# Performance work log

Hardware: AMD Instinct MI355X
Metric: run time of the kernel (lower is better)

Reference implementation:

```python
import jax, jax.numpy as jnp
import numpy as np

N_NODES = 50000


def sage_conv(x, src, dst, Wl, bl, Wr):
    # PyG SAGEConv (aggr='mean'): out = lin_l(mean_{j in N(i)} x_j) + lin_r(x_i)
    # lin_l has bias, lin_r (root) has no bias.
    n = x.shape[0]
    agg = jax.ops.segment_sum(x[src], dst, num_segments=n)          # [N, d_in]
    cnt = jax.ops.segment_sum(jnp.ones((src.shape[0],), x.dtype), dst, num_segments=n)
    mean = agg / jnp.maximum(cnt, 1.0)[:, None]
    return mean @ Wl + bl + x @ Wr


def setup_inputs() -> dict:
    key = jax.random.key(0)
    k1, k2, k3, k4, k5, k6, k7 = jax.random.split(key, 7)
    in_c, hid_c, out_c = 128, 128, 2
    x = jax.random.normal(k1, (N_NODES, in_c), dtype=jnp.float32)
    edge_index = jax.random.randint(k2, (2, 800000), 0, N_NODES, dtype=jnp.int64)
    s1 = 1.0 / np.sqrt(in_c)
    s2 = 1.0 / np.sqrt(hid_c)
    return {
        "x": x,
        "edge_index": edge_index,
        "W1l": jax.random.uniform(k3, (in_c, hid_c), jnp.float32, -s1, s1),
        "b1l": jnp.zeros((hid_c,), jnp.float32),
        "W1r": jax.random.uniform(k4, (in_c, hid_c), jnp.float32, -s1, s1),
        "W2l": jax.random.uniform(k5, (hid_c, out_c), jnp.float32, -s2, s2),
        "b2l": jnp.zeros((out_c,), jnp.float32),
        "W2r": jax.random.uniform(k6, (hid_c, out_c), jnp.float32, -s2, s2),
    }


def reference(x, edge_index, W1l, b1l, W1r, W2l, b2l, W2r):
    src, dst = edge_index[0], edge_index[1]
    h = jax.nn.relu(sage_conv(x, src, dst, W1l, b1l, W1r))
    return sage_conv(h, src, dst, W2l, b2l, W2r)
```

## Files before the change

### kernel.cpp

```cpp
#include <hip/hip_runtime.h>

#define N_NODES 50000
#define N_PAD 50176
#define N_EDGES 800000
#define C 128
#define CAP 48
#define NB 196
#define CBCAP 4608
#define B1_BUCK 391
#define TOBF_B 6250
#define PACK_B 16

typedef unsigned short ushort_t;
typedef unsigned int uint_t;
typedef __attribute__((ext_vector_type(8))) short bf16x8;
typedef __attribute__((ext_vector_type(4))) float f32x4;

__device__ __forceinline__ uint_t f2bf(float f) {
    uint_t u = __float_as_uint(f);
    u += 0x7fffu + ((u >> 16) & 1u);
    return u >> 16;
}
__device__ __forceinline__ float bflo(uint_t u) { return __uint_as_float(u << 16); }
__device__ __forceinline__ float bfhi(uint_t u) { return __uint_as_float(u & 0xffff0000u); }

__global__ __launch_bounds__(256) void bucket1_kernel(
    const int* __restrict__ src, const int* __restrict__ dst,
    int* __restrict__ gcur, int2* __restrict__ cb,
    const float* __restrict__ x, ushort_t* __restrict__ xh) {
    int b = blockIdx.x;
    if (b < B1_BUCK) {
        __shared__ int hist[NB];
        __shared__ int offs[NB];
        int t = threadIdx.x;
        if (t < NB) hist[t] = 0;
        __syncthreads();
        int tid = b * 256 + t;
        bool act = tid < N_EDGES / 8;
        int4 s0, s1, d0, d1;
        if (act) {
            s0 = ((const int4*)src)[2 * tid];
            s1 = ((const int4*)src)[2 * tid + 1];
            d0 = ((const int4*)dst)[2 * tid];
            d1 = ((const int4*)dst)[2 * tid + 1];
            atomicAdd(&hist[d0.x >> 8], 1);
            atomicAdd(&hist[d0.y >> 8], 1);
            atomicAdd(&hist[d0.z >> 8], 1);
            atomicAdd(&hist[d0.w >> 8], 1);
            atomicAdd(&hist[d1.x >> 8], 1);
            atomicAdd(&hist[d1.y >> 8], 1);
            atomicAdd(&hist[d1.z >> 8], 1);
            atomicAdd(&hist[d1.w >> 8], 1);
        }
        __syncthreads();
        if (t < NB) {
            offs[t] = atomicAdd(&gcur[t], hist[t]);
            hist[t] = 0;
        }
        __syncthreads();
        if (act) {
            int ss[8] = {s0.x, s0.y, s0.z, s0.w, s1.x, s1.y, s1.z, s1.w};
            int dd[8] = {d0.x, d0.y, d0.z, d0.w, d1.x, d1.y, d1.z, d1.w};
            #pragma unroll
            for (int i = 0; i < 8; i++) {
                int bkt = dd[i] >> 8;
                int pos = offs[bkt] + atomicAdd(&hist[bkt], 1);
                if (pos < CBCAP) cb[bkt * CBCAP + pos] = make_int2(ss[i], dd[i]);
            }
        }
    } else {
        int i = (b - B1_BUCK) * 256 + threadIdx.x;
        float4 v = ((const float4*)x)[i];
        uint_t lo = f2bf(v.x) | (f2bf(v.y) << 16);
        uint_t hi = f2bf(v.z) | (f2bf(v.w) << 16);
        ((uint2*)xh)[i] = make_uint2(lo, hi);
    }
}

__global__ __launch_bounds__(256) void bucket2_kernel(
    const int* __restrict__ gcur, const int2* __restrict__ cb,
    int* __restrict__ cursor, int* __restrict__ epad,
    const float* __restrict__ W1l, const float* __restrict__ W1r,
    ushort_t* __restrict__ Bp) {
    int b = blockIdx.x;
    if (b < NB) {
        __shared__ int cnt[256];
        int t = threadIdx.x;
        cnt[t] = 0;
        __syncthreads();
        int lenr = gcur[b];
        int len = lenr < CBCAP ? lenr : CBCAP;
        const int2* run = cb + b * CBCAP;
        for (int e = t; e < len; e += 256) {
            int2 sd = run[e];
            int pos = atomicAdd(&cnt[sd.y & 255], 1);
            if (pos < CAP) epad[sd.y * CAP + pos] = sd.x;
        }
        __syncthreads();
        int node = b * 256 + t;
        if (node < N_NODES) cursor[node] = cnt[t];
    } else {
        int p = (b - NB) * 256 + threadIdx.x;
        int lane = p & 63;
        int pair = p >> 6;
        int kk = pair & 7;
        int nt = pair >> 3;
        int n = lane & 15, quad = lane >> 4;
        int col = nt * 16 + n;
        int k0 = kk * 32 + quad * 8;
        uint_t w[4];
        #pragma unroll
        for (int jj = 0; jj < 4; jj++) {
            int ka = k0 + 2 * jj, kb = k0 + 2 * jj + 1;
            float fa = (ka < C) ? W1l[ka * C + col] : W1r[(ka - C) * C + col];
            float fb = (kb < C) ? W1l[kb * C + col] : W1r[(kb - C) * C + col];
            w[jj] = f2bf(fa) | (f2bf(fb) << 16);
        }
        ((uint4*)(Bp + (size_t)p * 8))[0] = make_uint4(w[0], w[1], w[2], w[3]);
    }
}

__device__ __forceinline__ void bf8_acc(float* a, const uint4 v) {
    a[0] += bflo(v.x); a[1] += bfhi(v.x);
    a[2] += bflo(v.y); a[3] += bfhi(v.y);
    a[4] += bflo(v.z); a[5] += bfhi(v.z);
    a[6] += bflo(v.w); a[7] += bfhi(v.w);
}

__global__ __launch_bounds__(256) void gather_kernel(const ushort_t* __restrict__ xh,
                                                     const int* __restrict__ cursor,
                                                     const int* __restrict__ epad,
                                                     ushort_t* __restrict__ msb) {
    int t = threadIdx.x;
    int slot = t >> 4, q = t & 15;
    int node = blockIdx.x * 16 + slot;
    int d = cursor[node];
    int dd = d < CAP ? d : CAP;
    const int* lst = epad + node * CAP;
    float a[8] = {0,0,0,0,0,0,0,0};
    float b[8] = {0,0,0,0,0,0,0,0};
    int e = 0;
    for (; e + 8 <= dd; e += 8) {
        int s0 = lst[e + 0], s1 = lst[e + 1], s2 = lst[e + 2], s3 = lst[e + 3];
        int s4 = lst[e + 4], s5 = lst[e + 5], s6 = lst[e + 6], s7 = lst[e + 7];
        uint4 v0 = ((const uint4*)(xh + (size_t)s0 * C))[q];
        uint4 v1 = ((const uint4*)(xh + (size_t)s1 * C))[q];
        uint4 v2 = ((const uint4*)(xh + (size_t)s2 * C))[q];
        uint4 v3 = ((const uint4*)(xh + (size_t)s3 * C))[q];
        uint4 v4 = ((const uint4*)(xh + (size_t)s4 * C))[q];
        uint4 v5 = ((const uint4*)(xh + (size_t)s5 * C))[q];
        uint4 v6 = ((const uint4*)(xh + (size_t)s6 * C))[q];
        uint4 v7 = ((const uint4*)(xh + (size_t)s7 * C))[q];
        bf8_acc(a, v0); bf8_acc(b, v1); bf8_acc(a, v2); bf8_acc(b, v3);
        bf8_acc(a, v4); bf8_acc(b, v5); bf8_acc(a, v6); bf8_acc(b, v7);
    }
    for (; e + 4 <= dd; e += 4) {
        int s0 = lst[e + 0], s1 = lst[e + 1], s2 = lst[e + 2], s3 = lst[e + 3];
        uint4 v0 = ((const uint4*)(xh + (size_t)s0 * C))[q];
        uint4 v1 = ((const uint4*)(xh + (size_t)s1 * C))[q];
        uint4 v2 = ((const uint4*)(xh + (size_t)s2 * C))[q];
        uint4 v3 = ((const uint4*)(xh + (size_t)s3 * C))[q];
        bf8_acc(a, v0); bf8_acc(b, v1); bf8_acc(a, v2); bf8_acc(b, v3);
    }
    for (; e < dd; e++) {
        uint4 v = ((const uint4*)(xh + (size_t)lst[e] * C))[q];
        bf8_acc(a, v);
    }
    float inv = 1.0f / fmaxf((float)d, 1.0f);
    uint4 o;
    o.x = f2bf((a[0] + b[0]) * inv) | (f2bf((a[1] + b[1]) * inv) << 16);
    o.y = f2bf((a[2] + b[2]) * inv) | (f2bf((a[3] + b[3]) * inv) << 16);
    o.z = f2bf((a[4] + b[4]) * inv) | (f2bf((a[5] + b[5]) * inv) << 16);
    o.w = f2bf((a[6] + b[6]) * inv) | (f2bf((a[7] + b[7]) * inv) << 16);
    ((uint4*)(msb + (size_t)node * C))[q] = o;
}

__global__ __launch_bounds__(512) void gemm_mfma(
    const ushort_t* __restrict__ msb, const ushort_t* __restrict__ xh,
    const ushort_t* __restrict__ Bp, const float* __restrict__ b1l,
    const float* __restrict__ W2l, const float* __restrict__ W2r,
    const float* __restrict__ b2l, float* __restrict__ z, float* __restrict__ out) {
    __shared__ ushort_t sB[2 * C * C];
    int t = threadIdx.x;
    #pragma unroll
    for (int i = 0; i < 8; i++)
        ((uint4*)sB)[i * 512 + t] = ((const uint4*)Bp)[i * 512 + t];
    __syncthreads();

    int wid = t >> 6, lane = t & 63;
    int m = lane & 15, quad = lane >> 4;
    int base = blockIdx.x * 128 + wid * 16;

    const ushort_t* a_ms = msb + (size_t)(base + m) * C + quad * 8;
    const ushort_t* a_xh = xh  + (size_t)(base + m) * C + quad * 8;
    bf16x8 aw[8];
    #pragma unroll
    for (int kk = 0; kk < 4; kk++) aw[kk]     = *(const bf16x8*)(a_ms + kk * 32);
    #pragma unroll
    for (int kk = 0; kk < 4; kk++) aw[4 + kk] = *(const bf16x8*)(a_xh + kk * 32);

    f32x4 acc[8];
    #pragma unroll
    for (int nt = 0; nt < 8; nt++) acc[nt] = (f32x4){0.f, 0.f, 0.f, 0.f};

    const bf16x8* bp = (const bf16x8*)sB;
    #pragma unroll
    for (int kk = 0; kk < 8; kk++) {
        bf16x8 a = aw[kk];
        #pragma unroll
        for (int nt = 0; nt < 8; nt++) {
            bf16x8 bfr = bp[(nt * 8 + kk) * 64 + lane];
            acc[nt] = __builtin_amdgcn_mfma_f32_16x16x32_bf16(a, bfr, acc[nt], 0, 0, 0);
        }
    }

    float zz0[4] = {0,0,0,0}, zz1[4] = {0,0,0,0};
    float rr0[4] = {0,0,0,0}, rr1[4] = {0,0,0,0};
    #pragma unroll
    for (int nt = 0; nt < 8; nt++) {
        int col = nt * 16 + m;
        float bias = b1l[col];
        float2 wl = ((const float2*)W2l)[col];
        float2 wr = ((const float2*)W2r)[col];
        #pragma unroll
        for (int reg = 0; reg < 4; reg++) {
            float h = fmaxf(acc[nt][reg] + bias, 0.0f);
            zz0[reg] = fmaf(h, wl.x, zz0[reg]);
            zz1[reg] = fmaf(h, wl.y, zz1[reg]);
            rr0[reg] = fmaf(h, wr.x, rr0[reg]);
            rr1[reg] = fmaf(h, wr.y, rr1[reg]);
        }
    }
    float bl0 = b2l[0], bl1 = b2l[1];
    #pragma unroll
    for (int reg = 0; reg < 4; reg++) {
        float a0 = zz0[reg], a1 = zz1[reg], c0 = rr0[reg], c1 = rr1[reg];
        #pragma unroll
        for (int off = 8; off > 0; off >>= 1) {
            a0 += __shfl_down(a0, off, 16);
            a1 += __shfl_down(a1, off, 16);
            c0 += __shfl_down(c0, off, 16);
            c1 += __shfl_down(c1, off, 16);
        }
        if (m == 0) {
            int node = base + quad * 4 + reg;
            if (node < N_NODES) {
                z[node * 2 + 0]   = a0;
                z[node * 2 + 1]   = a1;
                out[node * 2 + 0] = c0 + bl0;
                out[node * 2 + 1] = c1 + bl1;
            }
        }
    }
}

__global__ __launch_bounds__(256) void final_kernel(const float* __restrict__ z,
                                                    const int* __restrict__ cursor,
                                                    const int* __restrict__ epad,
                                                    float* __restrict__ out) {
    int t = threadIdx.x;
    int sub = t & 15;
    int node = blockIdx.x * 16 + (t >> 4);
    int d = cursor[node];
    int dd = d < CAP ? d : CAP;
    const int* lst = epad + node * CAP;
    float a0 = 0.0f, a1 = 0.0f;
    for (int e = sub; e < dd; e += 16) {
        float2 v = ((const float2*)z)[lst[e]];
        a0 += v.x; a1 += v.y;
    }
    #pragma unroll
    for (int off = 8; off > 0; off >>= 1) {
        a0 += __shfl_down(a0, off);
        a1 += __shfl_down(a1, off);
    }
    if (sub == 0) {
        float inv = 1.0f / fmaxf((float)d, 1.0f);
        out[node * 2 + 0] += a0 * inv;
        out[node * 2 + 1] += a1 * inv;
    }
}

extern "C" void kernel_launch(void* const* d_in, const int* in_sizes, int n_in,
                              void* d_out, int out_size, void* d_ws, size_t ws_size,
                              hipStream_t stream) {
    const float* x   = (const float*)d_in[0];
    const int*   ei  = (const int*)d_in[1];
    const float* W1l = (const float*)d_in[2];
    const float* b1l = (const float*)d_in[3];
    const float* W1r = (const float*)d_in[4];
    const float* W2l = (const float*)d_in[5];
    const float* b2l = (const float*)d_in[6];
    const float* W2r = (const float*)d_in[7];
    float* out = (float*)d_out;

    const int* src = ei;
    const int* dst = ei + N_EDGES;

    int* gcur     = (int*)d_ws;
    int2* cb      = (int2*)(gcur + 256);
    int* cursor   = (int*)(cb + NB * CBCAP);
    int* epad     = cursor + N_PAD;
    ushort_t* xh  = (ushort_t*)(epad + N_NODES * CAP);
    ushort_t* msb = xh + (size_t)N_PAD * C;
    ushort_t* Bp  = msb + (size_t)N_PAD * C;
    float* z      = (float*)(Bp + 2 * C * C);

    hipMemsetAsync(gcur, 0, NB * sizeof(int), stream);

    bucket1_kernel<<<B1_BUCK + TOBF_B, 256, 0, stream>>>(src, dst, gcur, cb, x, xh);
    bucket2_kernel<<<NB + PACK_B, 256, 0, stream>>>(gcur, cb, cursor, epad, W1l, W1r, Bp);
    gather_kernel<<<N_NODES / 16, 256, 0, stream>>>(xh, cursor, epad, msb);
    gemm_mfma<<<392, 512, 0, stream>>>(msb, xh, Bp, b1l, W2l, W2r, b2l, z, out);
    final_kernel<<<N_NODES / 16, 256, 0, stream>>>(z, cursor, epad, out);
}
```

Baseline: 158.2 us.

## Fuse neighbor mean-gather into MFMA GEMM kernel and widen bucket2 blocks

Removes the separate gather kernel and its bf16 intermediate buffer. Each GEMM lane now accumulates its node's neighbor rows directly into registers, converts them to bf16 A fragments, and overlaps the shared-memory B load with the gather before the barrier. bucket2 moves to 512-thread blocks with half the pack blocks. The cost is much lower memory-level parallelism in the gather (392 blocks, 16 lanes per node touching strided 16-byte chunks) and higher register pressure under a 4-wave occupancy hint.

```diff
diff --git a/kernel.cpp b/kernel.cpp
--- a/kernel.cpp
+++ b/kernel.cpp
@@ -9,7 +9,7 @@
 #define CBCAP 4608
 #define B1_BUCK 391
 #define TOBF_B 6250
-#define PACK_B 16
+#define PACK_B 8
 
 typedef unsigned short ushort_t;
 typedef unsigned int uint_t;
@@ -77,7 +77,7 @@
     }
 }
 
-__global__ __launch_bounds__(256) void bucket2_kernel(
+__global__ __launch_bounds__(512) void bucket2_kernel(
     const int* __restrict__ gcur, const int2* __restrict__ cb,
     int* __restrict__ cursor, int* __restrict__ epad,
     const float* __restrict__ W1l, const float* __restrict__ W1r,
@@ -86,21 +86,23 @@
     if (b < NB) {
         __shared__ int cnt[256];
         int t = threadIdx.x;
-        cnt[t] = 0;
+        if (t < 256) cnt[t] = 0;
         __syncthreads();
         int lenr = gcur[b];
         int len = lenr < CBCAP ? lenr : CBCAP;
         const int2* run = cb + b * CBCAP;
-        for (int e = t; e < len; e += 256) {
+        for (int e = t; e < len; e += 512) {
             int2 sd = run[e];
             int pos = atomicAdd(&cnt[sd.y & 255], 1);
             if (pos < CAP) epad[sd.y * CAP + pos] = sd.x;
         }
         __syncthreads();
-        int node = b * 256 + t;
-        if (node < N_NODES) cursor[node] = cnt[t];
+        if (t < 256) {
+            int node = b * 256 + t;
+            if (node < N_NODES) cursor[node] = cnt[t];
+        }
     } else {
-        int p = (b - NB) * 256 + threadIdx.x;
+        int p = (b - NB) * 512 + threadIdx.x;
         int lane = p & 63;
         int pair = p >> 6;
         int kk = pair & 7;
@@ -127,56 +129,9 @@
     a[6] += bflo(v.w); a[7] += bfhi(v.w);
 }
 
-__global__ __launch_bounds__(256) void gather_kernel(const ushort_t* __restrict__ xh,
-                                                     const int* __restrict__ cursor,
-                                                     const int* __restrict__ epad,
-                                                     ushort_t* __restrict__ msb) {
-    int t = threadIdx.x;
-    int slot = t >> 4, q = t & 15;
-    int node = blockIdx.x * 16 + slot;
-    int d = cursor[node];
-    int dd = d < CAP ? d : CAP;
-    const int* lst = epad + node * CAP;
-    float a[8] = {0,0,0,0,0,0,0,0};
-    float b[8] = {0,0,0,0,0,0,0,0};
-    int e = 0;
-    for (; e + 8 <= dd; e += 8) {
-        int s0 = lst[e + 0], s1 = lst[e + 1], s2 = lst[e + 2], s3 = lst[e + 3];
-        int s4 = lst[e + 4], s5 = lst[e + 5], s6 = lst[e + 6], s7 = lst[e + 7];
-        uint4 v0 = ((const uint4*)(xh + (size_t)s0 * C))[q];
-        uint4 v1 = ((const uint4*)(xh + (size_t)s1 * C))[q];
-        uint4 v2 = ((const uint4*)(xh + (size_t)s2 * C))[q];
-        uint4 v3 = ((const uint4*)(xh + (size_t)s3 * C))[q];
-        uint4 v4 = ((const uint4*)(xh + (size_t)s4 * C))[q];
-        uint4 v5 = ((const uint4*)(xh + (size_t)s5 * C))[q];
-        uint4 v6 = ((const uint4*)(xh + (size_t)s6 * C))[q];
-        uint4 v7 = ((const uint4*)(xh + (size_t)s7 * C))[q];
-        bf8_acc(a, v0); bf8_acc(b, v1); bf8_acc(a, v2); bf8_acc(b, v3);
-        bf8_acc(a, v4); bf8_acc(b, v5); bf8_acc(a, v6); bf8_acc(b, v7);
-    }
-    for (; e + 4 <= dd; e += 4) {
-        int s0 = lst[e + 0], s1 = lst[e + 1], s2 = lst[e + 2], s3 = lst[e + 3];
-        uint4 v0 = ((const uint4*)(xh + (size_t)s0 * C))[q];
-        uint4 v1 = ((const uint4*)(xh + (size_t)s1 * C))[q];
-        uint4 v2 = ((const uint4*)(xh + (size_t)s2 * C))[q];
-        uint4 v3 = ((const uint4*)(xh + (size_t)s3 * C))[q];
-        bf8_acc(a, v0); bf8_acc(b, v1); bf8_acc(a, v2); bf8_acc(b, v3);
-    }
-    for (; e < dd; e++) {
-        uint4 v = ((const uint4*)(xh + (size_t)lst[e] * C))[q];
-        bf8_acc(a, v);
-    }
-    float inv = 1.0f / fmaxf((float)d, 1.0f);
-    uint4 o;
-    o.x = f2bf((a[0] + b[0]) * inv) | (f2bf((a[1] + b[1]) * inv) << 16);
-    o.y = f2bf((a[2] + b[2]) * inv) | (f2bf((a[3] + b[3]) * inv) << 16);
-    o.z = f2bf((a[4] + b[4]) * inv) | (f2bf((a[5] + b[5]) * inv) << 16);
-    o.w = f2bf((a[6] + b[6]) * inv) | (f2bf((a[7] + b[7]) * inv) << 16);
-    ((uint4*)(msb + (size_t)node * C))[q] = o;
-}
-
-__global__ __launch_bounds__(512) void gemm_mfma(
-    const ushort_t* __restrict__ msb, const ushort_t* __restrict__ xh,
+__global__ __launch_bounds__(512, 4) void gemm_fused(
+    const ushort_t* __restrict__ xh,
+    const int* __restrict__ cursor, const int* __restrict__ epad,
     const ushort_t* __restrict__ Bp, const float* __restrict__ b1l,
     const float* __restrict__ W2l, const float* __restrict__ W2r,
     const float* __restrict__ b2l, float* __restrict__ z, float* __restrict__ out) {
@@ -185,19 +140,58 @@
     #pragma unroll
     for (int i = 0; i < 8; i++)
         ((uint4*)sB)[i * 512 + t] = ((const uint4*)Bp)[i * 512 + t];
-    __syncthreads();
 
     int wid = t >> 6, lane = t & 63;
     int m = lane & 15, quad = lane >> 4;
     int base = blockIdx.x * 128 + wid * 16;
-
-    const ushort_t* a_ms = msb + (size_t)(base + m) * C + quad * 8;
-    const ushort_t* a_xh = xh  + (size_t)(base + m) * C + quad * 8;
+    int node = base + m;
+
+    float ag[4][8];
+    #pragma unroll
+    for (int kk = 0; kk < 4; kk++)
+        #pragma unroll
+        for (int j = 0; j < 8; j++) ag[kk][j] = 0.0f;
+
+    int d = 0;
+    if (node < N_NODES) d = cursor[node];
+    int dd = d < CAP ? d : CAP;
+    const int* lst = epad + (size_t)node * CAP;
+
+    int e = 0;
+    for (; e + 2 <= dd; e += 2) {
+        int s0 = lst[e], s1 = lst[e + 1];
+        const uint4* r0 = (const uint4*)(xh + (size_t)s0 * C);
+        const uint4* r1 = (const uint4*)(xh + (size_t)s1 * C);
+        uint4 v00 = r0[quad], v01 = r0[4 + quad], v02 = r0[8 + quad], v03 = r0[12 + quad];
+        uint4 v10 = r1[quad], v11 = r1[4 + quad], v12 = r1[8 + quad], v13 = r1[12 + quad];
+        bf8_acc(ag[0], v00); bf8_acc(ag[1], v01); bf8_acc(ag[2], v02); bf8_acc(ag[3], v03);
+        bf8_acc(ag[0], v10); bf8_acc(ag[1], v11); bf8_acc(ag[2], v12); bf8_acc(ag[3], v13);
+    }
+    if (e < dd) {
+        int s0 = lst[e];
+        const uint4* r0 = (const uint4*)(xh + (size_t)s0 * C);
+        bf8_acc(ag[0], r0[quad]);
+        bf8_acc(ag[1], r0[4 + quad]);
+        bf8_acc(ag[2], r0[8 + quad]);
+        bf8_acc(ag[3], r0[12 + quad]);
+    }
+    float inv = 1.0f / fmaxf((float)d, 1.0f);
+
     bf16x8 aw[8];
     #pragma unroll
-    for (int kk = 0; kk < 4; kk++) aw[kk]     = *(const bf16x8*)(a_ms + kk * 32);
+    for (int kk = 0; kk < 4; kk++) {
+        uint4 u;
+        u.x = f2bf(ag[kk][0] * inv) | (f2bf(ag[kk][1] * inv) << 16);
+        u.y = f2bf(ag[kk][2] * inv) | (f2bf(ag[kk][3] * inv) << 16);
+        u.z = f2bf(ag[kk][4] * inv) | (f2bf(ag[kk][5] * inv) << 16);
+        u.w = f2bf(ag[kk][6] * inv) | (f2bf(ag[kk][7] * inv) << 16);
+        aw[kk] = *(bf16x8*)&u;
+    }
+    const ushort_t* a_xh = xh + (size_t)node * C + quad * 8;
     #pragma unroll
     for (int kk = 0; kk < 4; kk++) aw[4 + kk] = *(const bf16x8*)(a_xh + kk * 32);
+
+    __syncthreads();
 
     f32x4 acc[8];
     #pragma unroll
@@ -243,12 +237,12 @@
             c1 += __shfl_down(c1, off, 16);
         }
         if (m == 0) {
-            int node = base + quad * 4 + reg;
-            if (node < N_NODES) {
-                z[node * 2 + 0]   = a0;
-                z[node * 2 + 1]   = a1;
-                out[node * 2 + 0] = c0 + bl0;
-                out[node * 2 + 1] = c1 + bl1;
+            int onode = base + quad * 4 + reg;
+            if (onode < N_NODES) {
+                z[onode * 2 + 0]   = a0;
+                z[onode * 2 + 1]   = a1;
+                out[onode * 2 + 0] = c0 + bl0;
+                out[onode * 2 + 1] = c1 + bl1;
             }
         }
     }
@@ -302,15 +296,13 @@
     int* cursor   = (int*)(cb + NB * CBCAP);
     int* epad     = cursor + N_PAD;
     ushort_t* xh  = (ushort_t*)(epad + N_NODES * CAP);
-    ushort_t* msb = xh + (size_t)N_PAD * C;
-    ushort_t* Bp  = msb + (size_t)N_PAD * C;
+    ushort_t* Bp  = xh + (size_t)N_PAD * C;
     float* z      = (float*)(Bp + 2 * C * C);
 
     hipMemsetAsync(gcur, 0, NB * sizeof(int), stream);
 
     bucket1_kernel<<<B1_BUCK + TOBF_B, 256, 0, stream>>>(src, dst, gcur, cb, x, xh);
-    bucket2_kernel<<<NB + PACK_B, 256, 0, stream>>>(gcur, cb, cursor, epad, W1l, W1r, Bp);
-    gather_kernel<<<N_NODES / 16, 256, 0, stream>>>(xh, cursor, epad, msb);
-    gemm_mfma<<<392, 512, 0, stream>>>(msb, xh, Bp, b1l, W2l, W2r, b2l, z, out);
+    bucket2_kernel<<<NB + PACK_B, 512, 0, stream>>>(gcur, cb, cursor, epad, W1l, W1r, Bp);
+    gemm_fused<<<392, 512, 0, stream>>>(xh, cursor, epad, Bp, b1l, W2l, W2r, b2l, z, out);
     final_kernel<<<N_NODES / 16, 256, 0, stream>>>(z, cursor, epad, out);
 }
```

Result: no change. 161.0 us (+1.7%).
